# Kernel optimization log

Hardware: AMD Instinct MI355X
Metric: run time of the kernel (lower is better)

The kernel has to match this reference:

```python
import jax, jax.numpy as jnp
import numpy as np
from jax import lax

INPUT_DIM = 4
HIDDEN_DIM = 32
PRED_STEPS = 50
BATCH = 32768
SEQ_LEN = 200


def setup_inputs() -> dict:
    key = jax.random.key(0)
    ks = jax.random.split(key, 7)
    s = 1.0 / np.sqrt(HIDDEN_DIM)  # PyTorch LSTM init scale
    return {
        "history_data": jax.random.normal(ks[0], (BATCH, SEQ_LEN, INPUT_DIM), dtype=jnp.float32),
        "W_ih": jax.random.uniform(ks[1], (4 * HIDDEN_DIM, INPUT_DIM), jnp.float32, -s, s),
        "W_hh": jax.random.uniform(ks[2], (4 * HIDDEN_DIM, HIDDEN_DIM), jnp.float32, -s, s),
        "b_ih": jax.random.uniform(ks[3], (4 * HIDDEN_DIM,), jnp.float32, -s, s),
        "b_hh": jax.random.uniform(ks[4], (4 * HIDDEN_DIM,), jnp.float32, -s, s),
        "W_pred": jax.random.uniform(ks[5], (INPUT_DIM, HIDDEN_DIM), jnp.float32, -s, s),
        "b_pred": jax.random.uniform(ks[6], (INPUT_DIM,), jnp.float32, -s, s),
    }


def reference(history_data, W_ih, W_hh, b_ih, b_hh, W_pred, b_pred):
    H = W_hh.shape[1]
    b = b_ih + b_hh

    def cell(h, c, x):
        # PyTorch gate order: input, forget, cell(g), output
        gates = x @ W_ih.T + h @ W_hh.T + b  # [B, 4H]
        i, f, g, o = jnp.split(gates, 4, axis=-1)
        c_new = jax.nn.sigmoid(f) * c + jax.nn.sigmoid(i) * jnp.tanh(g)
        h_new = jax.nn.sigmoid(o) * jnp.tanh(c_new)
        return h_new, c_new

    B = history_data.shape[0]
    h0 = jnp.zeros((B, H), history_data.dtype)
    c0 = jnp.zeros((B, H), history_data.dtype)

    # Encode history: scan over time
    xs = jnp.swapaxes(history_data, 0, 1)  # [T, B, D]

    def hist_step(carry, x):
        h, c = carry
        h, c = cell(h, c, x)
        return (h, c), None

    (h, _), _ = lax.scan(hist_step, (h0, c0), xs)

    # each step (torch.zeros_like), carrying only h.
    def dec_step(h, _):
        pred = h @ W_pred.T + b_pred  # [B, INPUT_DIM]
        h_new, _ = cell(h, jnp.zeros_like(h), pred)
        return h_new, pred

    _, preds = lax.scan(dec_step, h, None, length=PRED_STEPS)  # [P, B, D]
    return jnp.swapaxes(preds, 0, 1)  # [B, PRED_STEPS, D]
```

## Files before the change

### kernel.cpp

```cpp
#include <hip/hip_runtime.h>
#include <math.h>

#define BATCH 32768
#define SEQLEN 200
#define PSTEPS 50
#define HID 32
#define LDS_PAD 36

typedef __attribute__((ext_vector_type(2))) _Float16 half2v;
typedef __attribute__((ext_vector_type(8))) _Float16 half8v;
typedef __attribute__((ext_vector_type(2))) __fp16   fp16x2;
typedef __attribute__((ext_vector_type(4))) float floatx4;
typedef __attribute__((ext_vector_type(2))) float float2v;

#define EXP2 __builtin_amdgcn_exp2f
#define RCPF __builtin_amdgcn_rcpf
#define PKRTZ __builtin_amdgcn_cvt_pkrtz
#define MED3 __builtin_amdgcn_fmed3f
#define FMA2 __builtin_elementwise_fma

#define L1C 1.4426950408889634f
#define L2C 2.8853900817779268f

union H8 { unsigned int u[4]; half8v h; half2v h2[4]; };
union HU { fp16x2 h; unsigned int u; };

__device__ __forceinline__ unsigned int pk(float a, float b) {
    HU t; t.h = PKRTZ(a, b); return t.u;
}

__global__ __launch_bounds__(256, 2)
void lstm_mfma_kernel(const float* __restrict__ hist, const float* __restrict__ W_ih,
                      const float* __restrict__ W_hh, const float* __restrict__ b_ih,
                      const float* __restrict__ b_hh, const float* __restrict__ W_pred,
                      const float* __restrict__ b_pred, float* __restrict__ out)
{
    const int lane = threadIdx.x & 63;
    const int wv   = threadIdx.x >> 6;
    const int m    = lane & 15;
    const int quad = lane >> 4;
    const int elem0 = (blockIdx.x * 4 + wv) * 16;

    if ((blockIdx.x >> 8) & 1) __builtin_amdgcn_s_sleep(12);

    __shared__ __align__(16) float h_lds_all[4][16][LDS_PAD];
    float (*hl)[LDS_PAD] = h_lds_all[wv];

    const float esc[4] = { -L1C, -L1C, L2C, -L1C };
    half8v Bh[8], B2[8];
    #pragma unroll
    for (int n = 0; n < 8; ++n) {
        const int gc = n * 16 + m;
        const float sc = esc[n >> 1];
        H8 bh;
        #pragma unroll
        for (int jj = 0; jj < 4; ++jj) {
            bh.h2[jj] = (half2v){ (_Float16)(sc * W_hh[gc * HID + quad * 8 + 2 * jj]),
                                  (_Float16)(sc * W_hh[gc * HID + quad * 8 + 2 * jj + 1]) };
        }
        Bh[n] = bh.h;
        H8 b2; b2.u[0] = b2.u[1] = b2.u[2] = b2.u[3] = 0u;
        if (quad == 0) {
            b2.h2[0] = (half2v){ (_Float16)(sc * W_ih[gc * 4 + 0]), (_Float16)(sc * W_ih[gc * 4 + 1]) };
            b2.h2[1] = (half2v){ (_Float16)(sc * W_ih[gc * 4 + 2]), (_Float16)(sc * W_ih[gc * 4 + 3]) };
            float bsum = sc * (b_ih[gc] + b_hh[gc]);
            _Float16 bhi = (_Float16)bsum;
            _Float16 blo = (_Float16)(bsum - (float)bhi);
            b2.h2[2] = (half2v){ bhi, blo };
        }
        B2[n] = b2.h;
    }
    const unsigned int one2 = 0x3C003C00u;
    const floatx4 zf4 = { 0.f, 0.f, 0.f, 0.f };

    float cst[2][4];
    #pragma unroll
    for (int hf = 0; hf < 2; ++hf)
        #pragma unroll
        for (int r = 0; r < 4; ++r) { cst[hf][r] = 0.f; hl[quad * 4 + r][hf * 16 + m] = 0.f; }

    const float4* xp = (const float4*)(hist + (size_t)(elem0 + m) * (SEQLEN * 4));
    float4 xv = xp[0];
    #pragma unroll 1
    for (int t = 0; t < SEQLEN; ++t) {
        float4 h0 = *(const float4*)&hl[m][quad * 8];
        float4 h1 = *(const float4*)&hl[m][quad * 8 + 4];
        H8 ahu;
        ahu.u[0] = pk(h0.x, h0.y); ahu.u[1] = pk(h0.z, h0.w);
        ahu.u[2] = pk(h1.x, h1.y); ahu.u[3] = pk(h1.z, h1.w);
        const half8v ah = ahu.h;

        const unsigned int tx0 = pk(xv.x, xv.y), tx1 = pk(xv.z, xv.w);
        H8 a2u;
        a2u.u[0] = (quad == 0) ? tx0 : 0u;
        a2u.u[1] = (quad == 0) ? tx1 : 0u;
        a2u.u[2] = (quad == 0) ? one2 : 0u;
        a2u.u[3] = 0u;
        const half8v a2 = a2u.h;

        const int tn = (t + 1 < SEQLEN) ? t + 1 : SEQLEN - 1;
        float4 xn = xp[tn];

        floatx4 acc[8];
        #pragma unroll
        for (int n = 0; n < 8; ++n) {
            floatx4 a = __builtin_amdgcn_mfma_f32_16x16x32_f16(a2, B2[n], zf4, 0, 0, 0);
            acc[n] = __builtin_amdgcn_mfma_f32_16x16x32_f16(ah, Bh[n], a, 0, 0, 0);
        }
        #pragma unroll
        for (int hf = 0; hf < 2; ++hf) {
            #pragma unroll
            for (int pr = 0; pr < 2; ++pr) {
                const int r0 = pr * 2, r1 = r0 + 1;
                const float2v ei = { EXP2(acc[0 + hf][r0]), EXP2(acc[0 + hf][r1]) };
                const float2v ef = { EXP2(acc[2 + hf][r0]), EXP2(acc[2 + hf][r1]) };
                const float2v eg = { EXP2(acc[4 + hf][r0]), EXP2(acc[4 + hf][r1]) };
                const float2v eo = { EXP2(acc[6 + hf][r0]), EXP2(acc[6 + hf][r1]) };
                const float2v pf = 1.f + ef;
                const float2v t1 = (1.f + ei) * (1.f + eg);
                const float2v cc = { cst[hf][r0], cst[hf][r1] };
                const float2v num = FMA2(cc, t1, (eg - 1.f) * pf);
                const float2v d  = t1 * pf;
                const float   R  = RCPF(d.x * d.y);
                const float2v dsw = { d.y, d.x };
                const float2v cn  = num * (R * dsw);
                const float2v cna = { MED3(cn.x, -12.f, 12.f), MED3(cn.y, -12.f, 12.f) };
                const float2v ea  = cna * L2C;
                const float2v ec  = { EXP2(ea.x), EXP2(ea.y) };
                const float2v dh  = (1.f + eo) * (1.f + ec);
                const float   Rh  = RCPF(dh.x * dh.y);
                const float2v dhsw = { dh.y, dh.x };
                const float2v hn  = (ec - 1.f) * (Rh * dhsw);

                cst[hf][r0] = cn.x; cst[hf][r1] = cn.y;
                hl[quad * 4 + r0][hf * 16 + m] = hn.x;
                hl[quad * 4 + r1][hf * 16 + m] = hn.y;
            }
        }
        xv = xn;
    }

    float wp[4][8];
    #pragma unroll
    for (int d = 0; d < 4; ++d)
        #pragma unroll
        for (int j = 0; j < 8; ++j) wp[d][j] = W_pred[d * HID + quad * 8 + j];
    float bp[4] = { b_pred[0], b_pred[1], b_pred[2], b_pred[3] };

    float* op = out + (size_t)(elem0 + m) * (PSTEPS * 4);
    #pragma unroll 1
    for (int p = 0; p < PSTEPS; ++p) {
        float4 h0 = *(const float4*)&hl[m][quad * 8];
        float4 h1 = *(const float4*)&hl[m][quad * 8 + 4];
        const float hv[8] = { h0.x, h0.y, h0.z, h0.w, h1.x, h1.y, h1.z, h1.w };

        float pd[4];
        #pragma unroll
        for (int d = 0; d < 4; ++d) {
            float s = 0.f;
            #pragma unroll
            for (int j = 0; j < 8; ++j) s = fmaf(hv[j], wp[d][j], s);
            s += __shfl_xor(s, 16);
            s += __shfl_xor(s, 32);
            pd[d] = s + bp[d];
        }
        if (quad == 0) *(float4*)(op + p * 4) = make_float4(pd[0], pd[1], pd[2], pd[3]);

        if (p + 1 < PSTEPS) {
            H8 ahu;
            ahu.u[0] = pk(hv[0], hv[1]); ahu.u[1] = pk(hv[2], hv[3]);
            ahu.u[2] = pk(hv[4], hv[5]); ahu.u[3] = pk(hv[6], hv[7]);
            const half8v ah = ahu.h;
            const unsigned int tx0 = pk(pd[0], pd[1]), tx1 = pk(pd[2], pd[3]);
            H8 a2u;
            a2u.u[0] = (quad == 0) ? tx0 : 0u;
            a2u.u[1] = (quad == 0) ? tx1 : 0u;
            a2u.u[2] = (quad == 0) ? one2 : 0u;
            a2u.u[3] = 0u;
            const half8v a2 = a2u.h;

            floatx4 acc[6];
            #pragma unroll
            for (int nn = 0; nn < 6; ++nn) {
                const int n = (nn < 2) ? nn : nn + 2;
                floatx4 a = __builtin_amdgcn_mfma_f32_16x16x32_f16(a2, B2[n], zf4, 0, 0, 0);
                acc[nn] = __builtin_amdgcn_mfma_f32_16x16x32_f16(ah, Bh[n], a, 0, 0, 0);
            }
            #pragma unroll
            for (int hf = 0; hf < 2; ++hf) {
                #pragma unroll
                for (int pr = 0; pr < 2; ++pr) {
                    const int r0 = pr * 2, r1 = r0 + 1;
                    const float2v ei = { EXP2(acc[0 + hf][r0]), EXP2(acc[0 + hf][r1]) };
                    const float2v eg = { EXP2(acc[2 + hf][r0]), EXP2(acc[2 + hf][r1]) };
                    const float2v eo = { EXP2(acc[4 + hf][r0]), EXP2(acc[4 + hf][r1]) };
                    const float2v d  = (1.f + ei) * (1.f + eg);
                    const float   R  = RCPF(d.x * d.y);
                    const float2v dsw = { d.y, d.x };
                    const float2v cn  = (eg - 1.f) * (R * dsw);
                    const float2v ea  = cn * L2C;
                    const float2v ec  = { EXP2(ea.x), EXP2(ea.y) };
                    const float2v dh  = (1.f + eo) * (1.f + ec);
                    const float   Rh  = RCPF(dh.x * dh.y);
                    const float2v dhsw = { dh.y, dh.x };
                    const float2v hn  = (ec - 1.f) * (Rh * dhsw);

                    hl[quad * 4 + r0][hf * 16 + m] = hn.x;
                    hl[quad * 4 + r1][hf * 16 + m] = hn.y;
                }
            }
        }
    }
}

extern "C" void kernel_launch(void* const* d_in, const int* in_sizes, int n_in,
                              void* d_out, int out_size, void* d_ws, size_t ws_size,
                              hipStream_t stream) {
    const float* hist   = (const float*)d_in[0];
    const float* W_ih   = (const float*)d_in[1];
    const float* W_hh   = (const float*)d_in[2];
    const float* b_ih   = (const float*)d_in[3];
    const float* b_hh   = (const float*)d_in[4];
    const float* W_pred = (const float*)d_in[5];
    const float* b_pred = (const float*)d_in[6];
    float* out = (float*)d_out;

    const int blocks = (BATCH / 16) / 4;
    lstm_mfma_kernel<<<blocks, 256, 0, stream>>>(hist, W_ih, W_hh, b_ih, b_hh,
                                                 W_pred, b_pred, out);
}
```

Baseline: 373.1 us.

## Transpose LSTM MFMA so hidden state stays in registers, removing LDS round-trip

Swaps the MFMA operand roles so the weight matrix is the A operand with a permuted row mapping, and the hidden state is the B operand. The gate outputs produced by each lane then line up with the B-operand layout the next step needs. This lets h be packed straight from registers into the next step's input and removes the per-step LDS store/load. The intent is to cut LDS traffic and its latency from the serial recurrence. Correctness depends on the phi0 row permutation matching the MFMA output and input layouts, and the W_pred dot product now reads the register-held h in that permuted order.

```diff
diff --git a/kernel.cpp b/kernel.cpp
--- a/kernel.cpp
+++ b/kernel.cpp
@@ -5,7 +5,6 @@
 #define SEQLEN 200
 #define PSTEPS 50
 #define HID 32
-#define LDS_PAD 36
 
 typedef __attribute__((ext_vector_type(2))) _Float16 half2v;
 typedef __attribute__((ext_vector_type(8))) _Float16 half8v;
@@ -43,70 +42,64 @@
 
     if ((blockIdx.x >> 8) & 1) __builtin_amdgcn_s_sleep(12);
 
-    __shared__ __align__(16) float h_lds_all[4][16][LDS_PAD];
-    float (*hl)[LDS_PAD] = h_lds_all[wv];
+    const int phi0 = ((m >> 2) * 8) + (m & 3);
 
     const float esc[4] = { -L1C, -L1C, L2C, -L1C };
-    half8v Bh[8], B2[8];
+    half8v Ah[8], Ax[8];
     #pragma unroll
-    for (int n = 0; n < 8; ++n) {
-        const int gc = n * 16 + m;
-        const float sc = esc[n >> 1];
-        H8 bh;
+    for (int T = 0; T < 8; ++T) {
+        const int g = T >> 1, hf = T & 1;
+        const int grow = g * 32 + phi0 + hf * 4;
+        const float sc = esc[g];
+        H8 ah;
         #pragma unroll
         for (int jj = 0; jj < 4; ++jj) {
-            bh.h2[jj] = (half2v){ (_Float16)(sc * W_hh[gc * HID + quad * 8 + 2 * jj]),
-                                  (_Float16)(sc * W_hh[gc * HID + quad * 8 + 2 * jj + 1]) };
-        }
-        Bh[n] = bh.h;
-        H8 b2; b2.u[0] = b2.u[1] = b2.u[2] = b2.u[3] = 0u;
+            ah.h2[jj] = (half2v){ (_Float16)(sc * W_hh[grow * HID + quad * 8 + 2 * jj]),
+                                  (_Float16)(sc * W_hh[grow * HID + quad * 8 + 2 * jj + 1]) };
+        }
+        Ah[T] = ah.h;
+        H8 ax; ax.u[0] = ax.u[1] = ax.u[2] = ax.u[3] = 0u;
         if (quad == 0) {
-            b2.h2[0] = (half2v){ (_Float16)(sc * W_ih[gc * 4 + 0]), (_Float16)(sc * W_ih[gc * 4 + 1]) };
-            b2.h2[1] = (half2v){ (_Float16)(sc * W_ih[gc * 4 + 2]), (_Float16)(sc * W_ih[gc * 4 + 3]) };
-            float bsum = sc * (b_ih[gc] + b_hh[gc]);
+            ax.h2[0] = (half2v){ (_Float16)(sc * W_ih[grow * 4 + 0]), (_Float16)(sc * W_ih[grow * 4 + 1]) };
+            ax.h2[1] = (half2v){ (_Float16)(sc * W_ih[grow * 4 + 2]), (_Float16)(sc * W_ih[grow * 4 + 3]) };
+            float bsum = sc * (b_ih[grow] + b_hh[grow]);
             _Float16 bhi = (_Float16)bsum;
             _Float16 blo = (_Float16)(bsum - (float)bhi);
-            b2.h2[2] = (half2v){ bhi, blo };
-        }
-        B2[n] = b2.h;
+            ax.h2[2] = (half2v){ bhi, blo };
+        }
+        Ax[T] = ax.h;
     }
     const unsigned int one2 = 0x3C003C00u;
     const floatx4 zf4 = { 0.f, 0.f, 0.f, 0.f };
 
-    float cst[2][4];
+    float cst[2][4], hr[2][4];
     #pragma unroll
     for (int hf = 0; hf < 2; ++hf)
         #pragma unroll
-        for (int r = 0; r < 4; ++r) { cst[hf][r] = 0.f; hl[quad * 4 + r][hf * 16 + m] = 0.f; }
+        for (int r = 0; r < 4; ++r) { cst[hf][r] = 0.f; hr[hf][r] = 0.f; }
+    H8 hb; hb.u[0] = hb.u[1] = hb.u[2] = hb.u[3] = 0u;
 
     const float4* xp = (const float4*)(hist + (size_t)(elem0 + m) * (SEQLEN * 4));
     float4 xv = xp[0];
     #pragma unroll 1
     for (int t = 0; t < SEQLEN; ++t) {
-        float4 h0 = *(const float4*)&hl[m][quad * 8];
-        float4 h1 = *(const float4*)&hl[m][quad * 8 + 4];
-        H8 ahu;
-        ahu.u[0] = pk(h0.x, h0.y); ahu.u[1] = pk(h0.z, h0.w);
-        ahu.u[2] = pk(h1.x, h1.y); ahu.u[3] = pk(h1.z, h1.w);
-        const half8v ah = ahu.h;
-
         const unsigned int tx0 = pk(xv.x, xv.y), tx1 = pk(xv.z, xv.w);
-        H8 a2u;
-        a2u.u[0] = (quad == 0) ? tx0 : 0u;
-        a2u.u[1] = (quad == 0) ? tx1 : 0u;
-        a2u.u[2] = (quad == 0) ? one2 : 0u;
-        a2u.u[3] = 0u;
-        const half8v a2 = a2u.h;
+        H8 bx;
+        bx.u[0] = (quad == 0) ? tx0 : 0u;
+        bx.u[1] = (quad == 0) ? tx1 : 0u;
+        bx.u[2] = (quad == 0) ? one2 : 0u;
+        bx.u[3] = 0u;
 
         const int tn = (t + 1 < SEQLEN) ? t + 1 : SEQLEN - 1;
         float4 xn = xp[tn];
 
         floatx4 acc[8];
         #pragma unroll
-        for (int n = 0; n < 8; ++n) {
-            floatx4 a = __builtin_amdgcn_mfma_f32_16x16x32_f16(a2, B2[n], zf4, 0, 0, 0);
-            acc[n] = __builtin_amdgcn_mfma_f32_16x16x32_f16(ah, Bh[n], a, 0, 0, 0);
-        }
+        for (int T = 0; T < 8; ++T) {
+            floatx4 a = __builtin_amdgcn_mfma_f32_16x16x32_f16(Ax[T], bx.h, zf4, 0, 0, 0);
+            acc[T] = __builtin_amdgcn_mfma_f32_16x16x32_f16(Ah[T], hb.h, a, 0, 0, 0);
+        }
+        H8 nhb;
         #pragma unroll
         for (int hf = 0; hf < 2; ++hf) {
             #pragma unroll
@@ -133,33 +126,30 @@
                 const float2v hn  = (ec - 1.f) * (Rh * dhsw);
 
                 cst[hf][r0] = cn.x; cst[hf][r1] = cn.y;
-                hl[quad * 4 + r0][hf * 16 + m] = hn.x;
-                hl[quad * 4 + r1][hf * 16 + m] = hn.y;
+                hr[hf][r0] = hn.x;  hr[hf][r1] = hn.y;
+                nhb.u[hf * 2 + pr] = pk(hn.x, hn.y);
             }
         }
+        hb = nhb;
         xv = xn;
     }
 
-    float wp[4][8];
+    float wpl[4][8];
     #pragma unroll
     for (int d = 0; d < 4; ++d)
         #pragma unroll
-        for (int j = 0; j < 8; ++j) wp[d][j] = W_pred[d * HID + quad * 8 + j];
+        for (int j = 0; j < 8; ++j) wpl[d][j] = W_pred[d * HID + quad * 8 + j];
     float bp[4] = { b_pred[0], b_pred[1], b_pred[2], b_pred[3] };
 
     float* op = out + (size_t)(elem0 + m) * (PSTEPS * 4);
     #pragma unroll 1
     for (int p = 0; p < PSTEPS; ++p) {
-        float4 h0 = *(const float4*)&hl[m][quad * 8];
-        float4 h1 = *(const float4*)&hl[m][quad * 8 + 4];
-        const float hv[8] = { h0.x, h0.y, h0.z, h0.w, h1.x, h1.y, h1.z, h1.w };
-
         float pd[4];
         #pragma unroll
         for (int d = 0; d < 4; ++d) {
             float s = 0.f;
             #pragma unroll
-            for (int j = 0; j < 8; ++j) s = fmaf(hv[j], wp[d][j], s);
+            for (int j = 0; j < 8; ++j) s = fmaf(hr[j >> 2][j & 3], wpl[d][j], s);
             s += __shfl_xor(s, 16);
             s += __shfl_xor(s, 32);
             pd[d] = s + bp[d];
@@ -167,25 +157,21 @@
         if (quad == 0) *(float4*)(op + p * 4) = make_float4(pd[0], pd[1], pd[2], pd[3]);
 
         if (p + 1 < PSTEPS) {
-            H8 ahu;
-            ahu.u[0] = pk(hv[0], hv[1]); ahu.u[1] = pk(hv[2], hv[3]);
-            ahu.u[2] = pk(hv[4], hv[5]); ahu.u[3] = pk(hv[6], hv[7]);
-            const half8v ah = ahu.h;
             const unsigned int tx0 = pk(pd[0], pd[1]), tx1 = pk(pd[2], pd[3]);
-            H8 a2u;
-            a2u.u[0] = (quad == 0) ? tx0 : 0u;
-            a2u.u[1] = (quad == 0) ? tx1 : 0u;
-            a2u.u[2] = (quad == 0) ? one2 : 0u;
-            a2u.u[3] = 0u;
-            const half8v a2 = a2u.h;
+            H8 bx;
+            bx.u[0] = (quad == 0) ? tx0 : 0u;
+            bx.u[1] = (quad == 0) ? tx1 : 0u;
+            bx.u[2] = (quad == 0) ? one2 : 0u;
+            bx.u[3] = 0u;
 
             floatx4 acc[6];
             #pragma unroll
             for (int nn = 0; nn < 6; ++nn) {
                 const int n = (nn < 2) ? nn : nn + 2;
-                floatx4 a = __builtin_amdgcn_mfma_f32_16x16x32_f16(a2, B2[n], zf4, 0, 0, 0);
-                acc[nn] = __builtin_amdgcn_mfma_f32_16x16x32_f16(ah, Bh[n], a, 0, 0, 0);
+                floatx4 a = __builtin_amdgcn_mfma_f32_16x16x32_f16(Ax[n], bx.h, zf4, 0, 0, 0);
+                acc[nn] = __builtin_amdgcn_mfma_f32_16x16x32_f16(Ah[n], hb.h, a, 0, 0, 0);
             }
+            H8 nhb;
             #pragma unroll
             for (int hf = 0; hf < 2; ++hf) {
                 #pragma unroll
@@ -205,10 +191,11 @@
                     const float2v dhsw = { dh.y, dh.x };
                     const float2v hn  = (ec - 1.f) * (Rh * dhsw);
 
-                    hl[quad * 4 + r0][hf * 16 + m] = hn.x;
-                    hl[quad * 4 + r1][hf * 16 + m] = hn.y;
+                    hr[hf][r0] = hn.x;  hr[hf][r1] = hn.y;
+                    nhb.u[hf * 2 + pr] = pk(hn.x, hn.y);
                 }
             }
+            hb = nhb;
         }
     }
 }
```

Measured after the change: 403.2 us. 1.08x slower.

## Split each 16-row tile's hidden units across two waves with double-buffered LDS

Applied to the files above, without the earlier changes.

Each block now handles one 16-element batch tile with two waves, and each wave computes half of the hidden units (4 gate tiles instead of 8). The new h is exchanged through a double-buffered LDS array with a __syncthreads per timestep. This halves the per-wave MFMA and transcendental work on the serial recurrence, aiming to cut per-step latency. The cost is twice as many waves for the same batch and a block barrier on every step. The staggered s_sleep is removed and launch bounds change to 128 threads with 4 blocks.

```diff
diff --git a/kernel.cpp b/kernel.cpp
--- a/kernel.cpp
+++ b/kernel.cpp
@@ -29,36 +29,33 @@
     HU t; t.h = PKRTZ(a, b); return t.u;
 }
 
-__global__ __launch_bounds__(256, 2)
+__global__ __launch_bounds__(128, 4)
 void lstm_mfma_kernel(const float* __restrict__ hist, const float* __restrict__ W_ih,
                       const float* __restrict__ W_hh, const float* __restrict__ b_ih,
                       const float* __restrict__ b_hh, const float* __restrict__ W_pred,
                       const float* __restrict__ b_pred, float* __restrict__ out)
 {
     const int lane = threadIdx.x & 63;
-    const int wv   = threadIdx.x >> 6;
+    const int hfw  = threadIdx.x >> 6;
     const int m    = lane & 15;
     const int quad = lane >> 4;
-    const int elem0 = (blockIdx.x * 4 + wv) * 16;
-
-    if ((blockIdx.x >> 8) & 1) __builtin_amdgcn_s_sleep(12);
-
-    __shared__ __align__(16) float h_lds_all[4][16][LDS_PAD];
-    float (*hl)[LDS_PAD] = h_lds_all[wv];
+    const int elem0 = blockIdx.x * 16;
+
+    __shared__ __align__(16) float hbuf[2][16][LDS_PAD];
 
     const float esc[4] = { -L1C, -L1C, L2C, -L1C };
-    half8v Bh[8], B2[8];
+    half8v Bh[4], B2[4];
     #pragma unroll
-    for (int n = 0; n < 8; ++n) {
-        const int gc = n * 16 + m;
-        const float sc = esc[n >> 1];
+    for (int g = 0; g < 4; ++g) {
+        const int gc = (2 * g + hfw) * 16 + m;
+        const float sc = esc[g];
         H8 bh;
         #pragma unroll
         for (int jj = 0; jj < 4; ++jj) {
             bh.h2[jj] = (half2v){ (_Float16)(sc * W_hh[gc * HID + quad * 8 + 2 * jj]),
                                   (_Float16)(sc * W_hh[gc * HID + quad * 8 + 2 * jj + 1]) };
         }
-        Bh[n] = bh.h;
+        Bh[g] = bh.h;
         H8 b2; b2.u[0] = b2.u[1] = b2.u[2] = b2.u[3] = 0u;
         if (quad == 0) {
             b2.h2[0] = (half2v){ (_Float16)(sc * W_ih[gc * 4 + 0]), (_Float16)(sc * W_ih[gc * 4 + 1]) };
@@ -68,23 +65,30 @@
             _Float16 blo = (_Float16)(bsum - (float)bhi);
             b2.h2[2] = (half2v){ bhi, blo };
         }
-        B2[n] = b2.h;
+        B2[g] = b2.h;
     }
     const unsigned int one2 = 0x3C003C00u;
     const floatx4 zf4 = { 0.f, 0.f, 0.f, 0.f };
 
-    float cst[2][4];
+    float cst[4];
     #pragma unroll
-    for (int hf = 0; hf < 2; ++hf)
-        #pragma unroll
-        for (int r = 0; r < 4; ++r) { cst[hf][r] = 0.f; hl[quad * 4 + r][hf * 16 + m] = 0.f; }
-
+    for (int r = 0; r < 4; ++r) {
+        cst[r] = 0.f;
+        hbuf[0][quad * 4 + r][hfw * 16 + m] = 0.f;
+        hbuf[1][quad * 4 + r][hfw * 16 + m] = 0.f;
+    }
+    __syncthreads();
+
+    int p = 0;
     const float4* xp = (const float4*)(hist + (size_t)(elem0 + m) * (SEQLEN * 4));
     float4 xv = xp[0];
     #pragma unroll 1
     for (int t = 0; t < SEQLEN; ++t) {
-        float4 h0 = *(const float4*)&hl[m][quad * 8];
-        float4 h1 = *(const float4*)&hl[m][quad * 8 + 4];
+        const int tn = (t + 1 < SEQLEN) ? t + 1 : SEQLEN - 1;
+        float4 xn = xp[tn];
+
+        float4 h0 = *(const float4*)&hbuf[p][m][quad * 8];
+        float4 h1 = *(const float4*)&hbuf[p][m][quad * 8 + 4];
         H8 ahu;
         ahu.u[0] = pk(h0.x, h0.y); ahu.u[1] = pk(h0.z, h0.w);
         ahu.u[2] = pk(h1.x, h1.y); ahu.u[3] = pk(h1.z, h1.w);
@@ -98,45 +102,41 @@
         a2u.u[3] = 0u;
         const half8v a2 = a2u.h;
 
-        const int tn = (t + 1 < SEQLEN) ? t + 1 : SEQLEN - 1;
-        float4 xn = xp[tn];
-
-        floatx4 acc[8];
-        #pragma unroll
-        for (int n = 0; n < 8; ++n) {
-            floatx4 a = __builtin_amdgcn_mfma_f32_16x16x32_f16(a2, B2[n], zf4, 0, 0, 0);
-            acc[n] = __builtin_amdgcn_mfma_f32_16x16x32_f16(ah, Bh[n], a, 0, 0, 0);
-        }
-        #pragma unroll
-        for (int hf = 0; hf < 2; ++hf) {
-            #pragma unroll
-            for (int pr = 0; pr < 2; ++pr) {
-                const int r0 = pr * 2, r1 = r0 + 1;
-                const float2v ei = { EXP2(acc[0 + hf][r0]), EXP2(acc[0 + hf][r1]) };
-                const float2v ef = { EXP2(acc[2 + hf][r0]), EXP2(acc[2 + hf][r1]) };
-                const float2v eg = { EXP2(acc[4 + hf][r0]), EXP2(acc[4 + hf][r1]) };
-                const float2v eo = { EXP2(acc[6 + hf][r0]), EXP2(acc[6 + hf][r1]) };
-                const float2v pf = 1.f + ef;
-                const float2v t1 = (1.f + ei) * (1.f + eg);
-                const float2v cc = { cst[hf][r0], cst[hf][r1] };
-                const float2v num = FMA2(cc, t1, (eg - 1.f) * pf);
-                const float2v d  = t1 * pf;
-                const float   R  = RCPF(d.x * d.y);
-                const float2v dsw = { d.y, d.x };
-                const float2v cn  = num * (R * dsw);
-                const float2v cna = { MED3(cn.x, -12.f, 12.f), MED3(cn.y, -12.f, 12.f) };
-                const float2v ea  = cna * L2C;
-                const float2v ec  = { EXP2(ea.x), EXP2(ea.y) };
-                const float2v dh  = (1.f + eo) * (1.f + ec);
-                const float   Rh  = RCPF(dh.x * dh.y);
-                const float2v dhsw = { dh.y, dh.x };
-                const float2v hn  = (ec - 1.f) * (Rh * dhsw);
-
-                cst[hf][r0] = cn.x; cst[hf][r1] = cn.y;
-                hl[quad * 4 + r0][hf * 16 + m] = hn.x;
-                hl[quad * 4 + r1][hf * 16 + m] = hn.y;
-            }
-        }
+        floatx4 acc[4];
+        #pragma unroll
+        for (int g = 0; g < 4; ++g) {
+            floatx4 a = __builtin_amdgcn_mfma_f32_16x16x32_f16(a2, B2[g], zf4, 0, 0, 0);
+            acc[g] = __builtin_amdgcn_mfma_f32_16x16x32_f16(ah, Bh[g], a, 0, 0, 0);
+        }
+        #pragma unroll
+        for (int pr = 0; pr < 2; ++pr) {
+            const int r0 = pr * 2, r1 = r0 + 1;
+            const float2v ei = { EXP2(acc[0][r0]), EXP2(acc[0][r1]) };
+            const float2v ef = { EXP2(acc[1][r0]), EXP2(acc[1][r1]) };
+            const float2v eg = { EXP2(acc[2][r0]), EXP2(acc[2][r1]) };
+            const float2v eo = { EXP2(acc[3][r0]), EXP2(acc[3][r1]) };
+            const float2v pf = 1.f + ef;
+            const float2v t1 = (1.f + ei) * (1.f + eg);
+            const float2v cc = { cst[r0], cst[r1] };
+            const float2v num = FMA2(cc, t1, (eg - 1.f) * pf);
+            const float2v d  = t1 * pf;
+            const float   R  = RCPF(d.x * d.y);
+            const float2v dsw = { d.y, d.x };
+            const float2v cn  = num * (R * dsw);
+            const float2v cna = { MED3(cn.x, -12.f, 12.f), MED3(cn.y, -12.f, 12.f) };
+            const float2v ea  = cna * L2C;
+            const float2v ec  = { EXP2(ea.x), EXP2(ea.y) };
+            const float2v dh  = (1.f + eo) * (1.f + ec);
+            const float   Rh  = RCPF(dh.x * dh.y);
+            const float2v dhsw = { dh.y, dh.x };
+            const float2v hn  = (ec - 1.f) * (Rh * dhsw);
+
+            cst[r0] = cn.x; cst[r1] = cn.y;
+            hbuf[p ^ 1][quad * 4 + r0][hfw * 16 + m] = hn.x;
+            hbuf[p ^ 1][quad * 4 + r1][hfw * 16 + m] = hn.y;
+        }
+        __syncthreads();
+        p ^= 1;
         xv = xn;
     }
 
@@ -149,9 +149,9 @@
 
     float* op = out + (size_t)(elem0 + m) * (PSTEPS * 4);
     #pragma unroll 1
-    for (int p = 0; p < PSTEPS; ++p) {
-        float4 h0 = *(const float4*)&hl[m][quad * 8];
-        float4 h1 = *(const float4*)&hl[m][quad * 8 + 4];
+    for (int ps = 0; ps < PSTEPS; ++ps) {
+        float4 h0 = *(const float4*)&hbuf[p][m][quad * 8];
+        float4 h1 = *(const float4*)&hbuf[p][m][quad * 8 + 4];
         const float hv[8] = { h0.x, h0.y, h0.z, h0.w, h1.x, h1.y, h1.z, h1.w };
 
         float pd[4];
@@ -164,9 +164,9 @@
             s += __shfl_xor(s, 32);
             pd[d] = s + bp[d];
         }
-        if (quad == 0) *(float4*)(op + p * 4) = make_float4(pd[0], pd[1], pd[2], pd[3]);
-
-        if (p + 1 < PSTEPS) {
+        if (hfw == 0 && quad == 0) *(float4*)(op + ps * 4) = make_float4(pd[0], pd[1], pd[2], pd[3]);
+
+        if (ps + 1 < PSTEPS) {
             H8 ahu;
             ahu.u[0] = pk(hv[0], hv[1]); ahu.u[1] = pk(hv[2], hv[3]);
             ahu.u[2] = pk(hv[4], hv[5]); ahu.u[3] = pk(hv[6], hv[7]);
@@ -179,36 +179,38 @@
             a2u.u[3] = 0u;
             const half8v a2 = a2u.h;
 
-            floatx4 acc[6];
-            #pragma unroll
-            for (int nn = 0; nn < 6; ++nn) {
-                const int n = (nn < 2) ? nn : nn + 2;
-                floatx4 a = __builtin_amdgcn_mfma_f32_16x16x32_f16(a2, B2[n], zf4, 0, 0, 0);
-                acc[nn] = __builtin_amdgcn_mfma_f32_16x16x32_f16(ah, Bh[n], a, 0, 0, 0);
+            floatx4 acc3[3];
+            {
+                floatx4 a;
+                a = __builtin_amdgcn_mfma_f32_16x16x32_f16(a2, B2[0], zf4, 0, 0, 0);
+                acc3[0] = __builtin_amdgcn_mfma_f32_16x16x32_f16(ah, Bh[0], a, 0, 0, 0);
+                a = __builtin_amdgcn_mfma_f32_16x16x32_f16(a2, B2[2], zf4, 0, 0, 0);
+                acc3[1] = __builtin_amdgcn_mfma_f32_16x16x32_f16(ah, Bh[2], a, 0, 0, 0);
+                a = __builtin_amdgcn_mfma_f32_16x16x32_f16(a2, B2[3], zf4, 0, 0, 0);
+                acc3[2] = __builtin_amdgcn_mfma_f32_16x16x32_f16(ah, Bh[3], a, 0, 0, 0);
             }
             #pragma unroll
-            for (int hf = 0; hf < 2; ++hf) {
-                #pragma unroll
-                for (int pr = 0; pr < 2; ++pr) {
-                    const int r0 = pr * 2, r1 = r0 + 1;
-                    const float2v ei = { EXP2(acc[0 + hf][r0]), EXP2(acc[0 + hf][r1]) };
-                    const float2v eg = { EXP2(acc[2 + hf][r0]), EXP2(acc[2 + hf][r1]) };
-                    const float2v eo = { EXP2(acc[4 + hf][r0]), EXP2(acc[4 + hf][r1]) };
-                    const float2v d  = (1.f + ei) * (1.f + eg);
-                    const float   R  = RCPF(d.x * d.y);
-                    const float2v dsw = { d.y, d.x };
-                    const float2v cn  = (eg - 1.f) * (R * dsw);
-                    const float2v ea  = cn * L2C;
-                    const float2v ec  = { EXP2(ea.x), EXP2(ea.y) };
-                    const float2v dh  = (1.f + eo) * (1.f + ec);
-                    const float   Rh  = RCPF(dh.x * dh.y);
-                    const float2v dhsw = { dh.y, dh.x };
-                    const float2v hn  = (ec - 1.f) * (Rh * dhsw);
-
-                    hl[quad * 4 + r0][hf * 16 + m] = hn.x;
-                    hl[quad * 4 + r1][hf * 16 + m] = hn.y;
-                }
+            for (int pr = 0; pr < 2; ++pr) {
+                const int r0 = pr * 2, r1 = r0 + 1;
+                const float2v ei = { EXP2(acc3[0][r0]), EXP2(acc3[0][r1]) };
+                const float2v eg = { EXP2(acc3[1][r0]), EXP2(acc3[1][r1]) };
+                const float2v eo = { EXP2(acc3[2][r0]), EXP2(acc3[2][r1]) };
+                const float2v d  = (1.f + ei) * (1.f + eg);
+                const float   R  = RCPF(d.x * d.y);
+                const float2v dsw = { d.y, d.x };
+                const float2v cn  = (eg - 1.f) * (R * dsw);
+                const float2v ea  = cn * L2C;
+                const float2v ec  = { EXP2(ea.x), EXP2(ea.y) };
+                const float2v dh  = (1.f + eo) * (1.f + ec);
+                const float   Rh  = RCPF(dh.x * dh.y);
+                const float2v dhsw = { dh.y, dh.x };
+                const float2v hn  = (ec - 1.f) * (Rh * dhsw);
+
+                hbuf[p ^ 1][quad * 4 + r0][hfw * 16 + m] = hn.x;
+                hbuf[p ^ 1][quad * 4 + r1][hfw * 16 + m] = hn.y;
             }
+            __syncthreads();
+            p ^= 1;
         }
     }
 }
@@ -225,7 +227,7 @@
     const float* b_pred = (const float*)d_in[6];
     float* out = (float*)d_out;
 
-    const int blocks = (BATCH / 16) / 4;
-    lstm_mfma_kernel<<<blocks, 256, 0, stream>>>(hist, W_ih, W_hh, b_ih, b_hh,
+    const int blocks = BATCH / 16;
+    lstm_mfma_kernel<<<blocks, 128, 0, stream>>>(hist, W_ih, W_hh, b_ih, b_hh,
                                                  W_pred, b_pred, out);
 }
```

Result: slower. 399.1 us (+7.0%).
